# Kernel optimization log

Measured on AMD Instinct MI355X. Metric: run time of the kernel, lower is better.

Reference implementation:

```python
import jax, jax.numpy as jnp
import numpy as np
import math

H = 8
E = 512
D_K = E // H
NEG = -1000000000.0
# last (and only surviving) row of dist_bar: one threshold per head
DIST_BAR = np.array([0.2, 0.3, 0.4, 0.5, 0.6, 0.7, 0.8, 0.9], dtype=np.float32)


def setup_inputs() -> dict:
    key = jax.random.key(0)
    ks = jax.random.split(key, 12)
    B, N = 8, 1024
    s = 1.0 / math.sqrt(E)
    inp = {
        "query": jax.random.normal(ks[0], (B, N, E), jnp.float32),
        "key": jax.random.normal(ks[1], (B, N, E), jnp.float32),
        "value": jax.random.normal(ks[2], (B, N, E), jnp.float32),
        "dist": jax.random.uniform(ks[3], (B, 1, N, N), jnp.float32),
        "mask": jnp.ones((B, N, N), jnp.int32),
        "Wq": jax.random.normal(ks[4], (E, E), jnp.float32) * s,
        "bq": jnp.zeros((E,), jnp.float32),
        "Wk": jax.random.normal(ks[5], (E, E), jnp.float32) * s,
        "bk": jnp.zeros((E,), jnp.float32),
        "Wv": jax.random.normal(ks[6], (E, E), jnp.float32) * s,
        "bv": jnp.zeros((E,), jnp.float32),
        "Wo": jax.random.normal(ks[7], (E, E), jnp.float32) * s,
        "bo": jnp.zeros((E,), jnp.float32),
    }
    return inp


def reference(query, key, value, dist, mask, Wq, bq, Wk, bk, Wv, bv, Wo, bo):
    B, N, _ = query.shape
    # project and split heads: [B, H, N, D_K]
    def heads(x, W, b):
        return (x @ W.T + b).reshape(B, N, H, D_K).transpose(0, 2, 1, 3)
    q = heads(query, Wq, bq)
    k = heads(key, Wk, bk)
    v = heads(value, Wv, bv)
    scores = jnp.einsum("bhqd,bhkd->bhqk", q, k) / math.sqrt(D_K)
    # padding mask: [B,N,N] -> [B,1,N,N]
    scores = jnp.where(mask[:, None, :, :] == 0, NEG, scores)
    # per-head distance mask: dist [B,1,N,N] < thr[h] -> [B,H,N,N]
    thr = jnp.asarray(DIST_BAR)[None, :, None, None]
    dmask = dist < thr
    # first row/col (global atom) always attend
    dmask = dmask.at[:, :, 0, :].set(True).at[:, :, :, 0].set(True)
    scores = jnp.where(dmask, scores, NEG)
    p = jax.nn.softmax(scores, axis=-1)
    out = jnp.einsum("bhqk,bhkd->bhqd", p, v)  # [B,H,N,D_K]
    out = out.transpose(0, 2, 1, 3).reshape(B, N, H * D_K)
    return out @ Wo.T + bo
```

## Files before the change

### kernel.cpp

```cpp
#include <hip/hip_runtime.h>
#include <stdint.h>


typedef __attribute__((ext_vector_type(8))) short short8;
typedef __attribute__((ext_vector_type(4))) float floatx4;
typedef unsigned long long u64;

#define MFMA16(a, b, c) __builtin_amdgcn_mfma_f32_16x16x32_bf16((a), (b), (c), 0, 0, 0)
#define QSCALE 0.1803368801111362f

static __device__ __forceinline__ unsigned short f2bf(float f) {
  union { float f; unsigned u; } v; v.f = f;
  unsigned r = v.u + 0x7fffu + ((v.u >> 16) & 1u);
  return (unsigned short)(r >> 16);
}

static __device__ __forceinline__ void gload_lds16(const void* g, void* l) {
  __builtin_amdgcn_global_load_lds((const __attribute__((address_space(1))) unsigned int*)g,
                                   (__attribute__((address_space(3))) unsigned int*)l,
                                   16, 0, 0);
}
static __device__ __forceinline__ int xsw(int row) { return (row & 3) ^ ((row >> 2) & 3); }

__global__ void prep_kernel(const float* __restrict__ q, const float* __restrict__ k,
                            const float* __restrict__ v,
                            const float* __restrict__ wq, const float* __restrict__ wk,
                            const float* __restrict__ wv, const float* __restrict__ wo,
                            const float* __restrict__ dist, const int* __restrict__ mask,
                            unsigned short* __restrict__ qb, unsigned short* __restrict__ kb,
                            unsigned short* __restrict__ vb,
                            unsigned short* __restrict__ wq16, unsigned short* __restrict__ wk16,
                            unsigned short* __restrict__ wv16, unsigned short* __restrict__ wo16,
                            u64* __restrict__ bits) {
  int gb = blockIdx.x;
  if (gb < 13312) {
    int i = gb * 256 + threadIdx.x;
    const float* s; unsigned short* d; int loc;
    if (i < 3145728) {
      int w = i >> 20; loc = i & 1048575;
      s = (w == 0) ? q : (w == 1) ? k : v;
      d = (w == 0) ? qb : (w == 1) ? kb : vb;
    } else {
      int j = i - 3145728; int w = j >> 16; loc = j & 65535;
      s = (w == 0) ? wq : (w == 1) ? wk : (w == 2) ? wv : wo;
      d = (w == 0) ? wq16 : (w == 1) ? wk16 : (w == 2) ? wv16 : wo16;
    }
    float4 vv = ((const float4*)s)[loc];
    ushort4 o;
    o.x = f2bf(vv.x); o.y = f2bf(vv.y); o.z = f2bf(vv.z); o.w = f2bf(vv.w);
    ((ushort4*)d)[loc] = o;
  } else {
    int bx = gb - 13312;
    int ktp = bx & 1;
    int brg = bx >> 1;
    int bb = brg >> 5, rg = brg & 31;
    int kt = ktp * 4 + (threadIdx.x >> 6);
    int lane = threadIdx.x & 63;
    int qq = lane >> 4, cc = lane & 15;
    const float* db = dist + ((size_t)bb << 20);
    const int* mb = mask + ((size_t)bb << 20);
    unsigned lo[8] = {0, 0, 0, 0, 0, 0, 0, 0};
    unsigned hi[8] = {0, 0, 0, 0, 0, 0, 0, 0};
#pragma unroll
    for (int st = 0; st < 2; st++)
#pragma unroll
      for (int ci = 0; ci < 8; ci++) {
        int col = kt * 128 + ci * 16 + cc;
#pragma unroll
        for (int r = 0; r < 4; r++) {
          int row = rg * 32 + st * 16 + qq * 4 + r;
          float d = db[((size_t)row << 10) + col];
          int m = mb[((size_t)row << 10) + col];
          int code = (d >= 0.2f) + (d >= 0.3f) + (d >= 0.4f) + (d >= 0.5f) +
                     (d >= 0.6f) + (d >= 0.7f) + (d >= 0.8f) + (d >= 0.9f);
          if (row == 0 || col == 0) code = 0;
          if (m == 0) code = 9;
          unsigned ab = (0xFFu << code) & 0xFFu;
          int pos = ci * 4 + r;
#pragma unroll
          for (int h = 0; h < 8; h++) {
            unsigned bit = ((ab >> h) & 1u) << pos;
            if (st == 0) lo[h] |= bit; else hi[h] |= bit;
          }
        }
      }
    u64* wout = bits + (((size_t)brg * 8 + kt) * 64 + lane) * 8;
#pragma unroll
    for (int h = 0; h < 8; h++) wout[h] = (u64)lo[h] | ((u64)hi[h] << 32);
  }
}

__global__ __launch_bounds__(256) void qkv_gemm(
    const unsigned short* __restrict__ Xq, const unsigned short* __restrict__ Xk,
    const unsigned short* __restrict__ Xv,
    const unsigned short* __restrict__ Wqp, const unsigned short* __restrict__ Wkp,
    const unsigned short* __restrict__ Wvp,
    const float* __restrict__ bq, const float* __restrict__ bk, const float* __restrict__ bv,
    unsigned short* __restrict__ Qh, unsigned short* __restrict__ Kh,
    unsigned short* __restrict__ Vt) {
  const int z = blockIdx.z;
  const unsigned short* X = (z == 0) ? Xq : (z == 1) ? Xk : Xv;
  const unsigned short* W = (z == 0) ? Wqp : (z == 1) ? Wkp : Wvp;
  const float* bias = (z == 0) ? bq : (z == 1) ? bk : bv;
  unsigned short* O = (z == 0) ? Qh : (z == 1) ? Kh : Vt;

  __shared__ __align__(16) short Xs[128 * 32];
  __shared__ __align__(16) short Ws[128 * 32];
  const int tid = threadIdx.x;
  const int lane = tid & 63;
  const int wave = tid >> 6;
  const int c = lane & 15;
  const int q = lane >> 4;
  const int m0 = blockIdx.x * 128;
  const int n0 = blockIdx.y * 128;
  const int wr = (wave >> 1) * 64;
  const int wc = (wave & 1) * 64;

  floatx4 acc[4][4];
#pragma unroll
  for (int i = 0; i < 4; i++)
#pragma unroll
    for (int j = 0; j < 4; j++) acc[i][j] = (floatx4)(0.0f);

  for (int k0 = 0; k0 < 512; k0 += 32) {
    __syncthreads();
#pragma unroll
    for (int it = 0; it < 2; it++) {
      int slot = wave * 128 + it * 64 + lane;
      int row = slot >> 2, ch = slot & 3;
      int g = ch ^ xsw(row);
      gload_lds16(X + (size_t)(m0 + row) * 512 + k0 + g * 8, &Xs[(wave * 128 + it * 64) * 8]);
      gload_lds16(W + (size_t)(n0 + row) * 512 + k0 + g * 8, &Ws[(wave * 128 + it * 64) * 8]);
    }
    __syncthreads();

    const short* Pa = (z == 2) ? Xs : Ws;
    const short* Pb = (z == 2) ? Ws : Xs;
    short8 af[4], bfv[4];
#pragma unroll
    for (int i = 0; i < 4; i++) {
      int row = wr + i * 16 + c;
      af[i] = *(const short8*)(&Pa[row * 32 + (q ^ xsw(row)) * 8]);
    }
#pragma unroll
    for (int j = 0; j < 4; j++) {
      int row = wc + j * 16 + c;
      bfv[j] = *(const short8*)(&Pb[row * 32 + (q ^ xsw(row)) * 8]);
    }
#pragma unroll
    for (int i = 0; i < 4; i++)
#pragma unroll
      for (int j = 0; j < 4; j++)
        acc[i][j] = MFMA16(af[i], bfv[j], acc[i][j]);
  }

  if (z == 2) {
#pragma unroll
    for (int i = 0; i < 4; i++) {
      int gm0 = m0 + wr + i * 16 + q * 4;
      int b = gm0 >> 10, n = gm0 & 1023;
#pragma unroll
      for (int j = 0; j < 4; j++) {
        int gn = n0 + wc + j * 16 + c;
        float bb = bias[gn];
        int h = gn >> 6, d = gn & 63;
        ushort4 pk;
#pragma unroll
        for (int r = 0; r < 4; r++) pk[r] = f2bf(acc[i][j][r] + bb);
        *(ushort4*)(&Vt[(((size_t)(b * 8 + h) * 64 + d) << 10) + n]) = pk;
      }
    }
  } else {
    const float scale = (z == 0) ? QSCALE : 1.0f;
#pragma unroll
    for (int i = 0; i < 4; i++) {
      int f0 = n0 + wr + i * 16 + q * 4;
      float4 bb4 = *(const float4*)(bias + f0);
      int h = f0 >> 6, d0 = f0 & 63;
      float bbs[4] = {bb4.x, bb4.y, bb4.z, bb4.w};
#pragma unroll
      for (int j = 0; j < 4; j++) {
        int t = m0 + wc + j * 16 + c;
        int b = t >> 10, n = t & 1023;
        ushort4 pk;
#pragma unroll
        for (int r = 0; r < 4; r++) pk[r] = f2bf((acc[i][j][r] + bbs[r]) * scale);
        *(ushort4*)(&O[((((size_t)(b * 8 + h)) << 10) + n) * 64 + d0]) = pk;
      }
    }
  }
}

__global__ __launch_bounds__(256) void out_gemm(const unsigned short* __restrict__ A,
                                                const unsigned short* __restrict__ W,
                                                const float* __restrict__ bias,
                                                float* __restrict__ Out) {
  __shared__ __align__(16) short As[128 * 32];
  __shared__ __align__(16) short Bs[64 * 32];
  const int tid = threadIdx.x;
  const int lane = tid & 63;
  const int wave = tid >> 6;
  const int c = lane & 15;
  const int q = lane >> 4;
  const int m0 = blockIdx.x * 128;
  const int n0 = blockIdx.y * 64;
  const int wr = (wave >> 1) * 64;
  const int wc = (wave & 1) * 32;

  floatx4 acc[4][2];
#pragma unroll
  for (int i = 0; i < 4; i++)
#pragma unroll
    for (int j = 0; j < 2; j++) acc[i][j] = (floatx4)(0.0f);

  for (int k0 = 0; k0 < 512; k0 += 32) {
    __syncthreads();
#pragma unroll
    for (int it = 0; it < 2; it++) {
      int slot = wave * 128 + it * 64 + lane;
      int row = slot >> 2, ch = slot & 3;
      int g = ch ^ xsw(row);
      gload_lds16(A + (size_t)(m0 + row) * 512 + k0 + g * 8, &As[(wave * 128 + it * 64) * 8]);
    }
    {
      int slot = wave * 64 + lane;
      int row = slot >> 2, ch = slot & 3;
      int g = ch ^ xsw(row);
      gload_lds16(W + (size_t)(n0 + row) * 512 + k0 + g * 8, &Bs[(wave * 64) * 8]);
    }
    __syncthreads();

    short8 af[4], bfv[2];
#pragma unroll
    for (int i = 0; i < 4; i++) {
      int row = wr + i * 16 + c;
      af[i] = *(const short8*)(&As[row * 32 + (q ^ xsw(row)) * 8]);
    }
#pragma unroll
    for (int j = 0; j < 2; j++) {
      int row = wc + j * 16 + c;
      bfv[j] = *(const short8*)(&Bs[row * 32 + (q ^ xsw(row)) * 8]);
    }
#pragma unroll
    for (int i = 0; i < 4; i++)
#pragma unroll
      for (int j = 0; j < 2; j++)
        acc[i][j] = MFMA16(af[i], bfv[j], acc[i][j]);
  }

#pragma unroll
  for (int i = 0; i < 4; i++) {
    int gm0 = m0 + wr + i * 16 + q * 4;
#pragma unroll
    for (int j = 0; j < 2; j++) {
      int gn = n0 + wc + j * 16 + c;
      float bb = bias[gn];
#pragma unroll
      for (int r = 0; r < 4; r++)
        Out[(size_t)(gm0 + r) * 512 + gn] = acc[i][j][r] + bb;
    }
  }
}

__global__ __launch_bounds__(256) void attn_kernel(const unsigned short* __restrict__ Qh,
                                                   const unsigned short* __restrict__ Kh,
                                                   const unsigned short* __restrict__ Vt,
                                                   const u64* __restrict__ bits,
                                                   unsigned short* __restrict__ AO) {
  __shared__ __align__(16) unsigned short P[4][32 * 132];
  __shared__ float rsx[2][32];
  const int tid = threadIdx.x;
  const int lane = tid & 63;
  const int wave = tid >> 6;
  const int c = lane & 15;
  const int q = lane >> 4;
  const int bh = blockIdx.y;
  const int b = bh >> 3;
  const int h = bh & 7;
  const size_t base = (size_t)bh << 16;
  const int qc = wave >> 1;
  const int kvh = wave & 1;
  const int rbase = blockIdx.x * 64 + qc * 32;
  const int rg = rbase >> 5;
  unsigned short* Pw = &P[wave][0];

  short8 aq[2][2];
#pragma unroll
  for (int st = 0; st < 2; st++)
#pragma unroll
    for (int kk = 0; kk < 2; kk++)
      aq[st][kk] = *(const short8*)(Qh + base + (size_t)(rbase + st * 16 + c) * 64 + kk * 32 + q * 8);

  const u64* wb = bits + (((size_t)(b * 32 + rg) * 8) * 64 + lane) * 8 + h;
  const unsigned short* Kb = Kh + base;
  const unsigned short* Vb = Vt + base;

  float rs[2][4];
#pragma unroll
  for (int st = 0; st < 2; st++)
#pragma unroll
    for (int r = 0; r < 4; r++) rs[st][r] = 0.0f;
  floatx4 o[2][4];
#pragma unroll
  for (int st = 0; st < 2; st++)
#pragma unroll
    for (int ci = 0; ci < 4; ci++) o[st][ci] = (floatx4)(0.0f);

  for (int kt = kvh * 4; kt < kvh * 4 + 4; kt++) {
    const unsigned short* Kt = Kb + (size_t)kt * 128 * 64;
    u64 w64 = wb[(size_t)kt * 512];
    unsigned wlo = (unsigned)w64, whi = (unsigned)(w64 >> 32);
#pragma unroll
    for (int hf = 0; hf < 2; hf++) {
      floatx4 s[2][4];
#pragma unroll
      for (int c2 = 0; c2 < 4; c2++) { s[0][c2] = (floatx4)(0.0f); s[1][c2] = (floatx4)(0.0f); }
#pragma unroll
      for (int c2 = 0; c2 < 4; c2++) {
        int ci = hf * 4 + c2;
#pragma unroll
        for (int kk = 0; kk < 2; kk++) {
          short8 bk = *(const short8*)(Kt + (size_t)(ci * 16 + c) * 64 + kk * 32 + q * 8);
          s[0][c2] = MFMA16(aq[0][kk], bk, s[0][c2]);
          s[1][c2] = MFMA16(aq[1][kk], bk, s[1][c2]);
        }
      }
#pragma unroll
      for (int st = 0; st < 2; st++) {
        unsigned sel = st ? whi : wlo;
#pragma unroll
        for (int c2 = 0; c2 < 4; c2++) {
          int ci = hf * 4 + c2;
#pragma unroll
          for (int r = 0; r < 4; r++) {
            float e = ((sel >> (ci * 4 + r)) & 1u) ? exp2f(s[st][c2][r]) : 0.0f;
            rs[st][r] += e;
            Pw[(st * 16 + q * 4 + r) * 132 + ci * 16 + c] = f2bf(e);
          }
        }
      }
    }
#pragma unroll
    for (int ch = 0; ch < 4; ch++) {
      short8 ap0 = *(const short8*)(&Pw[(size_t)c * 132 + ch * 32 + q * 8]);
      short8 ap1 = *(const short8*)(&Pw[(size_t)(16 + c) * 132 + ch * 32 + q * 8]);
#pragma unroll
      for (int ci = 0; ci < 4; ci++) {
        short8 bv = *(const short8*)(Vb + (size_t)(ci * 16 + c) * 1024 + kt * 128 + ch * 32 + q * 8);
        o[0][ci] = MFMA16(ap0, bv, o[0][ci]);
        o[1][ci] = MFMA16(ap1, bv, o[1][ci]);
      }
    }
  }

#pragma unroll
  for (int st = 0; st < 2; st++)
#pragma unroll
    for (int r = 0; r < 4; r++) {
      float v = rs[st][r];
      v += __shfl_xor(v, 1); v += __shfl_xor(v, 2);
      v += __shfl_xor(v, 4); v += __shfl_xor(v, 8);
      rs[st][r] = v;
    }

  float* dump = (float*)&P[qc * 2 + 1][0];
  if (kvh == 1) {
#pragma unroll
    for (int st = 0; st < 2; st++)
#pragma unroll
      for (int ci = 0; ci < 4; ci++)
#pragma unroll
        for (int r = 0; r < 4; r++)
          dump[lane * 33 + (st * 4 + ci) * 4 + r] = o[st][ci][r];
    if (c == 0) {
#pragma unroll
      for (int st = 0; st < 2; st++)
#pragma unroll
        for (int r = 0; r < 4; r++) rsx[qc][st * 16 + q * 4 + r] = rs[st][r];
    }
  }
  __syncthreads();
  if (kvh == 0) {
    float inv[2][4];
#pragma unroll
    for (int st = 0; st < 2; st++)
#pragma unroll
      for (int ci = 0; ci < 4; ci++)
#pragma unroll
        for (int r = 0; r < 4; r++)
          o[st][ci][r] += dump[lane * 33 + (st * 4 + ci) * 4 + r];
#pragma unroll
    for (int st = 0; st < 2; st++)
#pragma unroll
      for (int r = 0; r < 4; r++)
        inv[st][r] = 1.0f / (rs[st][r] + rsx[qc][st * 16 + q * 4 + r]);
#pragma unroll
    for (int st = 0; st < 2; st++)
#pragma unroll
      for (int r = 0; r < 4; r++) {
        int n = rbase + st * 16 + q * 4 + r;
        size_t ob = ((size_t)((b << 10) + n)) * 512 + h * 64;
#pragma unroll
        for (int ci = 0; ci < 4; ci++)
          AO[ob + ci * 16 + c] = f2bf(o[st][ci][r] * inv[st][r]);
      }
  }
}

extern "C" void kernel_launch(void* const* d_in, const int* in_sizes, int n_in,
                              void* d_out, int out_size, void* d_ws, size_t ws_size,
                              hipStream_t stream) {
  const float* query = (const float*)d_in[0];
  const float* key_  = (const float*)d_in[1];
  const float* value = (const float*)d_in[2];
  const float* dist  = (const float*)d_in[3];
  const int*   mask  = (const int*)d_in[4];
  const float* Wq = (const float*)d_in[5];
  const float* bq = (const float*)d_in[6];
  const float* Wk = (const float*)d_in[7];
  const float* bk = (const float*)d_in[8];
  const float* Wv = (const float*)d_in[9];
  const float* bv = (const float*)d_in[10];
  const float* Wo = (const float*)d_in[11];
  const float* bo = (const float*)d_in[12];

  char* ws = (char*)d_ws;
  size_t off = 0;
  auto alloc = [&](size_t bytes) -> char* {
    char* p = ws + off;
    off += (bytes + 255) & ~(size_t)255;
    return p;
  };
  const size_t NQKV = 8192ull * 512;
  unsigned short* qb   = (unsigned short*)alloc(NQKV * 2);
  unsigned short* kb   = (unsigned short*)alloc(NQKV * 2);
  unsigned short* vb   = (unsigned short*)alloc(NQKV * 2);
  unsigned short* wq16 = (unsigned short*)alloc(512ull * 512 * 2);
  unsigned short* wk16 = (unsigned short*)alloc(512ull * 512 * 2);
  unsigned short* wv16 = (unsigned short*)alloc(512ull * 512 * 2);
  unsigned short* wo16 = (unsigned short*)alloc(512ull * 512 * 2);
  unsigned short* Qh = (unsigned short*)alloc(NQKV * 2);
  unsigned short* Kh = (unsigned short*)alloc(NQKV * 2);
  unsigned short* Vt = (unsigned short*)alloc(NQKV * 2);
  unsigned short* AO = (unsigned short*)alloc(NQKV * 2);
  u64*            bits = (u64*)alloc(8ull * 1024 * 1024);

  prep_kernel<<<13824, 256, 0, stream>>>(query, key_, value, Wq, Wk, Wv, Wo, dist, mask,
                                         qb, kb, vb, wq16, wk16, wv16, wo16, bits);
  qkv_gemm<<<dim3(64, 4, 3), 256, 0, stream>>>(qb, kb, vb, wq16, wk16, wv16,
                                               bq, bk, bv, Qh, Kh, Vt);
  attn_kernel<<<dim3(16, 64), 256, 0, stream>>>(Qh, Kh, Vt, bits, AO);
  out_gemm<<<dim3(64, 8), 256, 0, stream>>>(AO, wo16, bo, (float*)d_out);
}
```

Before: 332.9 us.

## Stage dist/mask through LDS with coalesced loads; widen attention blocks and prefetch V

The mask-bit builder now reads dist and mask for a 32-row band with coalesced float4/int4 loads. It packs per-element codes into a swizzled LDS tile and then builds the per-head bitmasks from LDS, one block per row group instead of two. This replaces the strided scalar global reads of the old path. The attention kernel goes to 512-thread blocks with 8 waves (128 query rows per block) and issues the first V chunk loads early so they overlap the QK^T and softmax work. The cost is more LDS per block for both kernels, which may lower occupancy.

Result: faster. 314.3 us (-5.6%).

```diff
diff --git a/kernel.cpp b/kernel.cpp
--- a/kernel.cpp
+++ b/kernel.cpp
@@ -32,6 +32,7 @@
                             unsigned short* __restrict__ wq16, unsigned short* __restrict__ wk16,
                             unsigned short* __restrict__ wv16, unsigned short* __restrict__ wo16,
                             u64* __restrict__ bits) {
+  __shared__ unsigned Ct[32 * 256];
   int gb = blockIdx.x;
   if (gb < 13312) {
     int i = gb * 256 + threadIdx.x;
@@ -50,43 +51,62 @@
     o.x = f2bf(vv.x); o.y = f2bf(vv.y); o.z = f2bf(vv.z); o.w = f2bf(vv.w);
     ((ushort4*)d)[loc] = o;
   } else {
-    int bx = gb - 13312;
-    int ktp = bx & 1;
-    int brg = bx >> 1;
+    int brg = gb - 13312;
     int bb = brg >> 5, rg = brg & 31;
-    int kt = ktp * 4 + (threadIdx.x >> 6);
-    int lane = threadIdx.x & 63;
+    int t = threadIdx.x;
+    const float* db = dist + ((size_t)bb << 20) + ((size_t)(rg * 32) << 10);
+    const int* mb = mask + ((size_t)bb << 20) + ((size_t)(rg * 32) << 10);
+#pragma unroll 4
+    for (int i = 0; i < 32; i++) {
+      int f4 = i * 256 + t;
+      float4 d4 = ((const float4*)db)[f4];
+      int4 m4 = ((const int4*)mb)[f4];
+      float dv[4] = {d4.x, d4.y, d4.z, d4.w};
+      int mv[4] = {m4.x, m4.y, m4.z, m4.w};
+      int grow = rg * 32 + i;
+      unsigned pk = 0;
+#pragma unroll
+      for (int u = 0; u < 4; u++) {
+        float d = dv[u];
+        int code = (d >= 0.2f) + (d >= 0.3f) + (d >= 0.4f) + (d >= 0.5f) +
+                   (d >= 0.6f) + (d >= 0.7f) + (d >= 0.8f) + (d >= 0.9f);
+        if (grow == 0 || (t * 4 + u) == 0) code = 0;
+        if (mv[u] == 0) code = 9;
+        pk |= ((unsigned)code) << (u * 8);
+      }
+      Ct[i * 256 + (t ^ (i & 12))] = pk;
+    }
+    __syncthreads();
+    int lane = t & 63;
+    int ktb = t >> 6;
     int qq = lane >> 4, cc = lane & 15;
-    const float* db = dist + ((size_t)bb << 20);
-    const int* mb = mask + ((size_t)bb << 20);
-    unsigned lo[8] = {0, 0, 0, 0, 0, 0, 0, 0};
-    unsigned hi[8] = {0, 0, 0, 0, 0, 0, 0, 0};
-#pragma unroll
-    for (int st = 0; st < 2; st++)
-#pragma unroll
-      for (int ci = 0; ci < 8; ci++) {
-        int col = kt * 128 + ci * 16 + cc;
-#pragma unroll
-        for (int r = 0; r < 4; r++) {
-          int row = rg * 32 + st * 16 + qq * 4 + r;
-          float d = db[((size_t)row << 10) + col];
-          int m = mb[((size_t)row << 10) + col];
-          int code = (d >= 0.2f) + (d >= 0.3f) + (d >= 0.4f) + (d >= 0.5f) +
-                     (d >= 0.6f) + (d >= 0.7f) + (d >= 0.8f) + (d >= 0.9f);
-          if (row == 0 || col == 0) code = 0;
-          if (m == 0) code = 9;
-          unsigned ab = (0xFFu << code) & 0xFFu;
-          int pos = ci * 4 + r;
-#pragma unroll
-          for (int h = 0; h < 8; h++) {
-            unsigned bit = ((ab >> h) & 1u) << pos;
-            if (st == 0) lo[h] |= bit; else hi[h] |= bit;
+#pragma unroll
+    for (int p = 0; p < 2; p++) {
+      int kt = ktb + p * 4;
+      unsigned lo[8] = {0, 0, 0, 0, 0, 0, 0, 0};
+      unsigned hi[8] = {0, 0, 0, 0, 0, 0, 0, 0};
+#pragma unroll
+      for (int st = 0; st < 2; st++)
+#pragma unroll
+        for (int ci = 0; ci < 8; ci++)
+#pragma unroll
+          for (int r = 0; r < 4; r++) {
+            int row = st * 16 + qq * 4 + r;
+            int col = kt * 128 + ci * 16 + cc;
+            unsigned w = Ct[row * 256 + (((col >> 2) ^ (row & 12)) & 255)];
+            int code = (w >> ((col & 3) * 8)) & 0xff;
+            unsigned ab = (0xFFu << code) & 0xFFu;
+            int pos = ci * 4 + r;
+#pragma unroll
+            for (int h = 0; h < 8; h++) {
+              unsigned bit = ((ab >> h) & 1u) << pos;
+              if (st == 0) lo[h] |= bit; else hi[h] |= bit;
+            }
           }
-        }
-      }
-    u64* wout = bits + (((size_t)brg * 8 + kt) * 64 + lane) * 8;
-#pragma unroll
-    for (int h = 0; h < 8; h++) wout[h] = (u64)lo[h] | ((u64)hi[h] << 32);
+      u64* wout = bits + (((size_t)brg * 8 + kt) * 64 + lane) * 8;
+#pragma unroll
+      for (int h = 0; h < 8; h++) wout[h] = (u64)lo[h] | ((u64)hi[h] << 32);
+    }
   }
 }
 
@@ -262,13 +282,13 @@
   }
 }
 
-__global__ __launch_bounds__(256) void attn_kernel(const unsigned short* __restrict__ Qh,
+__global__ __launch_bounds__(512) void attn_kernel(const unsigned short* __restrict__ Qh,
                                                    const unsigned short* __restrict__ Kh,
                                                    const unsigned short* __restrict__ Vt,
                                                    const u64* __restrict__ bits,
                                                    unsigned short* __restrict__ AO) {
-  __shared__ __align__(16) unsigned short P[4][32 * 132];
-  __shared__ float rsx[2][32];
+  __shared__ __align__(16) unsigned short P[8][32 * 132];
+  __shared__ float rsx[4][32];
   const int tid = threadIdx.x;
   const int lane = tid & 63;
   const int wave = tid >> 6;
@@ -280,7 +300,7 @@
   const size_t base = (size_t)bh << 16;
   const int qc = wave >> 1;
   const int kvh = wave & 1;
-  const int rbase = blockIdx.x * 64 + qc * 32;
+  const int rbase = blockIdx.x * 128 + qc * 32;
   const int rg = rbase >> 5;
   unsigned short* Pw = &P[wave][0];
 
@@ -310,6 +330,10 @@
     const unsigned short* Kt = Kb + (size_t)kt * 128 * 64;
     u64 w64 = wb[(size_t)kt * 512];
     unsigned wlo = (unsigned)w64, whi = (unsigned)(w64 >> 32);
+    short8 vf[4];
+#pragma unroll
+    for (int ci = 0; ci < 4; ci++)
+      vf[ci] = *(const short8*)(Vb + (size_t)(ci * 16 + c) * 1024 + kt * 128 + q * 8);
 #pragma unroll
     for (int hf = 0; hf < 2; hf++) {
       floatx4 s[2][4];
@@ -340,8 +364,17 @@
         }
       }
     }
-#pragma unroll
-    for (int ch = 0; ch < 4; ch++) {
+    {
+      short8 ap0 = *(const short8*)(&Pw[(size_t)c * 132 + q * 8]);
+      short8 ap1 = *(const short8*)(&Pw[(size_t)(16 + c) * 132 + q * 8]);
+#pragma unroll
+      for (int ci = 0; ci < 4; ci++) {
+        o[0][ci] = MFMA16(ap0, vf[ci], o[0][ci]);
+        o[1][ci] = MFMA16(ap1, vf[ci], o[1][ci]);
+      }
+    }
+#pragma unroll
+    for (int ch = 1; ch < 4; ch++) {
       short8 ap0 = *(const short8*)(&Pw[(size_t)c * 132 + ch * 32 + q * 8]);
       short8 ap1 = *(const short8*)(&Pw[(size_t)(16 + c) * 132 + ch * 32 + q * 8]);
 #pragma unroll
@@ -445,10 +478,10 @@
   unsigned short* AO = (unsigned short*)alloc(NQKV * 2);
   u64*            bits = (u64*)alloc(8ull * 1024 * 1024);
 
-  prep_kernel<<<13824, 256, 0, stream>>>(query, key_, value, Wq, Wk, Wv, Wo, dist, mask,
+  prep_kernel<<<13568, 256, 0, stream>>>(query, key_, value, Wq, Wk, Wv, Wo, dist, mask,
                                          qb, kb, vb, wq16, wk16, wv16, wo16, bits);
   qkv_gemm<<<dim3(64, 4, 3), 256, 0, stream>>>(qb, kb, vb, wq16, wk16, wv16,
                                                bq, bk, bv, Qh, Kh, Vt);
-  attn_kernel<<<dim3(16, 64), 256, 0, stream>>>(Qh, Kh, Vt, bits, AO);
+  attn_kernel<<<dim3(8, 64), 512, 0, stream>>>(Qh, Kh, Vt, bits, AO);
   out_gemm<<<dim3(64, 8), 256, 0, stream>>>(AO, wo16, bo, (float*)d_out);
 }
```
